# Performance work log

Measured on AMD Instinct MI355X. Metric: run time of the kernel, lower is better.

## Reference

```python
import jax, jax.numpy as jnp
import numpy as np

D_MODEL = 1024
N_HEADS = 16
HEAD_DIM = D_MODEL // N_HEADS


def setup_inputs() -> dict:
    key = jax.random.key(0)
    ks = jax.random.split(key, 5)
    q = jax.random.normal(ks[0], (2, 2048, D_MODEL), dtype=jnp.float32)
    Wq = jax.random.normal(ks[1], (D_MODEL, D_MODEL), dtype=jnp.float32) * (1.0 / np.sqrt(D_MODEL))
    bq = jax.random.normal(ks[2], (D_MODEL,), dtype=jnp.float32) * 0.01
    Wo = jax.random.normal(ks[3], (D_MODEL, D_MODEL), dtype=jnp.float32) * (1.0 / np.sqrt(D_MODEL))
    bo = jax.random.normal(ks[4], (D_MODEL,), dtype=jnp.float32) * 0.01
    return {"q": q, "Wq": Wq, "bq": bq, "Wo": Wo, "bo": bo}


def reference(q, Wq, bq, Wo, bo):
    bs, S, dim = q.shape
    # NOTE: original module (bug-faithfully) projects Q, K and V all with WQ.
    proj = q @ Wq.T + bq  # [B, S, D]
    h = proj.reshape(bs, S, N_HEADS, HEAD_DIM).transpose(0, 2, 1, 3)  # [B, H, S, Dh]
    qh, kh, vh = h, h, h
    scale = HEAD_DIM ** -0.5
    attn = jnp.einsum('bhqd,bhkd->bhqk', qh, kh) * scale  # [B, H, S, S]
    scores = jax.nn.softmax(attn, axis=-1)
    # dropout is identity in inference mode
    vals = jnp.einsum('bhqk,bhkd->bhqd', scores, vh)  # [B, H, S, Dh]
    vals = vals.transpose(0, 2, 1, 3).reshape(bs, S, dim)
    return vals @ Wo.T + bo
```

## Files before the change

### kernel.cpp

```cpp
#include <hip/hip_runtime.h>

#define D_MODEL 1024
#define N_HEADS 16
#define HEAD_DIM 64
#define SEQ 2048
#define BATCH 2
#define M_TOTAL (BATCH*SEQ)

typedef __bf16 bf16;
typedef __bf16 bf16x8 __attribute__((ext_vector_type(8)));
typedef __bf16 bf16x4 __attribute__((ext_vector_type(4)));
typedef float  floatx4 __attribute__((ext_vector_type(4)));

__device__ __forceinline__ void gl2lds16(const bf16* g, bf16* l) {
    __builtin_amdgcn_global_load_lds(
        (const __attribute__((address_space(1))) unsigned int*)g,
        (__attribute__((address_space(3))) unsigned int*)l, 16, 0, 0);
}

__global__ void cvt_all(const float* __restrict__ q, const float* __restrict__ Wq,
                        const float* __restrict__ Wo, bf16* __restrict__ qb,
                        bf16* __restrict__ wqb, bf16* __restrict__ wob) {
    int i = blockIdx.x * 256 + threadIdx.x;
    const float* src; bf16* dst; int off;
    if (i < 1048576)      { src = q;  dst = qb;  off = i; }
    else if (i < 1310720) { src = Wq; dst = wqb; off = i - 1048576; }
    else                  { src = Wo; dst = wob; off = i - 1310720; }
    float4 v = ((const float4*)src)[off];
    bf16x4 o;
    o[0] = (bf16)v.x; o[1] = (bf16)v.y; o[2] = (bf16)v.z; o[3] = (bf16)v.w;
    ((bf16x4*)dst)[off] = o;
}

template<int MODE>
__global__ __launch_bounds__(512)
void gemm_bt_bias_t(const bf16* __restrict__ A, const bf16* __restrict__ B,
                    const float* __restrict__ bias, void* __restrict__ Cout,
                    bf16* __restrict__ Cout2, int M, int N, int K)
{
    __shared__ __align__(16) bf16 As[2][128 * 32];
    __shared__ __align__(16) bf16 Bs[2][128 * 32];

    const int tid  = threadIdx.x;
    const int lane = tid & 63;
    const int wave = tid >> 6;
    const int quad = lane >> 4;
    const int l16  = lane & 15;
    const int m0   = blockIdx.y * 128;
    const int n0   = blockIdx.x * 128;
    const int wm   = (wave >> 2) * 64;
    const int wn   = (wave & 3) * 32;

    floatx4 acc[4][2];
#pragma unroll
    for (int i = 0; i < 4; i++)
#pragma unroll
        for (int j = 0; j < 2; j++) acc[i][j] = (floatx4){0.f, 0.f, 0.f, 0.f};

    const int srow = tid >> 2;
    const int sc   = (tid & 3) ^ ((srow >> 1) & 3);
    auto issue = [&](int buf, int k0) {
        gl2lds16(A + (size_t)(m0 + srow) * K + k0 + sc * 8, &As[buf][tid * 8]);
        gl2lds16(B + (size_t)(n0 + srow) * K + k0 + sc * 8, &Bs[buf][tid * 8]);
    };
    issue(0, 0);
    int buf = 0;
    for (int k0 = 0; k0 < K; k0 += 32, buf ^= 1) {
        __syncthreads();
        if (k0 + 32 < K) issue(buf ^ 1, k0 + 32);
        bf16x8 af[4], bfr[2];
#pragma unroll
        for (int i = 0; i < 4; i++) {
            int row = wm + i * 16 + l16;
            af[i] = *(const bf16x8*)&As[buf][row * 32 + ((quad ^ ((row >> 1) & 3)) * 8)];
        }
#pragma unroll
        for (int j = 0; j < 2; j++) {
            int row = wn + j * 16 + l16;
            bfr[j] = *(const bf16x8*)&Bs[buf][row * 32 + ((quad ^ ((row >> 1) & 3)) * 8)];
        }
#pragma unroll
        for (int i = 0; i < 4; i++)
#pragma unroll
            for (int j = 0; j < 2; j++)
                acc[i][j] = __builtin_amdgcn_mfma_f32_16x16x32_bf16(
                    af[i], bfr[j], acc[i][j], 0, 0, 0);
    }

    if constexpr (MODE == 0) {
        float* C = (float*)Cout;
#pragma unroll
        for (int j = 0; j < 2; j++) {
            int col  = n0 + wn + j * 16 + l16;
            float bv = bias[col];
#pragma unroll
            for (int i = 0; i < 4; i++) {
                int rbase = m0 + wm + i * 16 + quad * 4;
#pragma unroll
                for (int r = 0; r < 4; r++)
                    C[(size_t)(rbase + r) * N + col] = acc[i][j][r] + bv;
            }
        }
    } else {
        bf16* Cb = (bf16*)Cout;
#pragma unroll
        for (int j = 0; j < 2; j++) {
            int col = n0 + wn + j * 16 + l16;
            int h   = col >> 6, d = col & 63;
            float bv = bias[col];
#pragma unroll
            for (int i = 0; i < 4; i++) {
                int rbase = m0 + wm + i * 16 + quad * 4;
                int b  = rbase >> 11;
                int s0 = rbase & 2047;
                bf16x4 o4;
#pragma unroll
                for (int r = 0; r < 4; r++) {
                    float v = acc[i][j][r] + bv;
                    o4[r] = (bf16)v;
                    Cb[(((size_t)(b * N_HEADS + h) * SEQ + (s0 + r)) << 6) + d] = (bf16)v;
                }
                *(bf16x4*)&Cout2[((size_t)(b * N_HEADS + h) * 64 + d) * SEQ + s0] = o4;
            }
        }
    }
}

__global__ __launch_bounds__(256)
void flash_attn(const bf16* __restrict__ projbf, const bf16* __restrict__ projT,
                bf16* __restrict__ vals)
{
    __shared__ __align__(16) bf16 Ks[2][128 * 64];
    __shared__ __align__(16) bf16 Vt[2][64 * 128];
    __shared__ __align__(16) bf16 Pt[128 * 40];

    const int tid  = threadIdx.x;
    const int lane = tid & 63;
    const int wave = tid >> 6;
    const int quad = lane >> 4;
    const int l16  = lane & 15;
    const int q0   = blockIdx.x * 128;
    const int bh   = blockIdx.y;
    const bf16* hK  = projbf + (size_t)bh * SEQ * 64;
    const bf16* hVt = projT  + (size_t)bh * 64 * SEQ;
    const int wq0  = wave * 32;

    bf16x8 qf[2][2];
#pragma unroll
    for (int nb = 0; nb < 2; nb++)
#pragma unroll
        for (int ks = 0; ks < 2; ks++)
            qf[nb][ks] = *(const bf16x8*)(hK + (size_t)(q0 + wq0 + nb * 16 + l16) * 64
                                          + ks * 32 + quad * 8);

    floatx4 oacc[4][2];
#pragma unroll
    for (int mb = 0; mb < 4; mb++)
#pragma unroll
        for (int nb = 0; nb < 2; nb++) oacc[mb][nb] = (floatx4){0.f, 0.f, 0.f, 0.f};
    float lsum[2] = {0.f, 0.f};

    auto issue = [&](int buf, int k0) {
#pragma unroll
        for (int it = 0; it < 4; it++) {
            int row = it * 32 + (tid >> 3);
            int c   = (tid & 7) ^ (row & 7);
            gl2lds16(hK + (size_t)(k0 + row) * 64 + c * 8,
                     &Ks[buf][it * 2048 + tid * 8]);
        }
#pragma unroll
        for (int it = 0; it < 4; it++) {
            int row = it * 16 + (tid >> 4);
            int c   = (tid & 15) ^ (row & 15);
            gl2lds16(hVt + (size_t)row * SEQ + k0 + c * 8,
                     &Vt[buf][it * 2048 + tid * 8]);
        }
    };
    issue(0, 0);
    int buf = 0;
    for (int k0 = 0; k0 < SEQ; k0 += 128, buf ^= 1) {
        __syncthreads();
        if (k0 + 128 < SEQ) issue(buf ^ 1, k0 + 128);

#pragma unroll
        for (int ck = 0; ck < 4; ck++) {
#pragma unroll
            for (int kb = 0; kb < 2; kb++) {
                int krow = ck * 32 + kb * 16 + l16;
                bf16x8 kf0 = *(const bf16x8*)&Ks[buf][krow * 64 + ((quad ^ (krow & 7)) * 8)];
                bf16x8 kf1 = *(const bf16x8*)&Ks[buf][krow * 64 + (((4 + quad) ^ (krow & 7)) * 8)];
                floatx4 sacc[2];
#pragma unroll
                for (int nb = 0; nb < 2; nb++) {
                    sacc[nb] = __builtin_amdgcn_mfma_f32_16x16x32_bf16(
                        kf0, qf[nb][0], (floatx4){0.f, 0.f, 0.f, 0.f}, 0, 0, 0);
                    sacc[nb] = __builtin_amdgcn_mfma_f32_16x16x32_bf16(
                        kf1, qf[nb][1], sacc[nb], 0, 0, 0);
                }
#pragma unroll
                for (int nb = 0; nb < 2; nb++) {
                    bf16x4 p4; float ps = 0.f;
#pragma unroll
                    for (int r = 0; r < 4; r++) {
                        float p = __expf(sacc[nb][r] * 0.125f - 16.0f);
                        p4[r] = (bf16)p; ps += p;
                    }
                    lsum[nb] += ps;
                    *(bf16x4*)&Pt[(wq0 + nb * 16 + l16) * 40 + kb * 16 + quad * 4] = p4;
                }
            }
            bf16x8 pf[2];
#pragma unroll
            for (int nb = 0; nb < 2; nb++)
                pf[nb] = *(const bf16x8*)&Pt[(wq0 + nb * 16 + l16) * 40 + quad * 8];
#pragma unroll
            for (int mb = 0; mb < 4; mb++) {
                int vrow = mb * 16 + l16;
                bf16x8 vf = *(const bf16x8*)&Vt[buf][vrow * 128
                                                + (((ck * 4 + quad) ^ (vrow & 15)) * 8)];
#pragma unroll
                for (int nb = 0; nb < 2; nb++)
                    oacc[mb][nb] = __builtin_amdgcn_mfma_f32_16x16x32_bf16(
                        vf, pf[nb], oacc[mb][nb], 0, 0, 0);
            }
        }
    }

#pragma unroll
    for (int nb = 0; nb < 2; nb++) {
        lsum[nb] += __shfl_xor(lsum[nb], 16);
        lsum[nb] += __shfl_xor(lsum[nb], 32);
    }
    const int b = bh >> 4, h = bh & 15;
#pragma unroll
    for (int nb = 0; nb < 2; nb++) {
        float rinv = 1.0f / lsum[nb];
        int q = q0 + wq0 + nb * 16 + l16;
#pragma unroll
        for (int mb = 0; mb < 4; mb++) {
            bf16x4 o4;
#pragma unroll
            for (int r = 0; r < 4; r++) o4[r] = (bf16)(oacc[mb][nb][r] * rinv);
            *(bf16x4*)&vals[((size_t)b * SEQ + q) * D_MODEL + h * 64 + mb * 16 + quad * 4] = o4;
        }
    }
}

extern "C" void kernel_launch(void* const* d_in, const int* in_sizes, int n_in,
                              void* d_out, int out_size, void* d_ws, size_t ws_size,
                              hipStream_t stream)
{
    const float* q  = (const float*)d_in[0];
    const float* Wq = (const float*)d_in[1];
    const float* bq = (const float*)d_in[2];
    const float* Wo = (const float*)d_in[3];
    const float* bo = (const float*)d_in[4];
    float* out = (float*)d_out;

    char* ws = (char*)d_ws;
    bf16* qbf    = (bf16*)(ws);
    bf16* Wqbf   = (bf16*)(ws + (size_t)( 8 << 20));
    bf16* Wobf   = (bf16*)(ws + (size_t)(10 << 20));
    bf16* projbf = (bf16*)(ws + (size_t)(12 << 20));
    bf16* projT  = (bf16*)(ws + (size_t)(20 << 20));
    bf16* valsb  = (bf16*)(ws + (size_t)(28 << 20));

    cvt_all<<<6144, 256, 0, stream>>>(q, Wq, Wo, qbf, Wqbf, Wobf);

    gemm_bt_bias_t<1><<<dim3(8, 32), 512, 0, stream>>>(qbf, Wqbf, bq, (void*)projbf,
                                                       projT, M_TOTAL, D_MODEL, D_MODEL);

    flash_attn<<<dim3(SEQ / 128, BATCH * N_HEADS), 256, 0, stream>>>(projbf, projT, valsb);

    gemm_bt_bias_t<0><<<dim3(8, 32), 512, 0, stream>>>(valsb, Wobf, bo, (void*)out,
                                                       nullptr, M_TOTAL, D_MODEL, D_MODEL);
}
```

Before: 179.9 us.

## Stage transposed projection store through LDS and remap attention grid for L2 locality

The projection GEMM epilogue now writes the transposed V copy by first placing the tile in the shared memory buffer with an XOR swizzle, then emitting coalesced 16-byte row stores instead of strided 8-byte stores. The flash attention launch becomes a 1D grid whose block index is remapped so that blocks of the same head land on the same XCD under round-robin dispatch, improving L2 reuse of K/V. The epilogue adds two barriers and reuses the GEMM LDS buffers.

After: 170.6 us. 1.05x faster.

```diff
diff --git a/kernel.cpp b/kernel.cpp
--- a/kernel.cpp
+++ b/kernel.cpp
@@ -38,8 +38,9 @@
                     const float* __restrict__ bias, void* __restrict__ Cout,
                     bf16* __restrict__ Cout2, int M, int N, int K)
 {
-    __shared__ __align__(16) bf16 As[2][128 * 32];
-    __shared__ __align__(16) bf16 Bs[2][128 * 32];
+    __shared__ __align__(16) bf16 smem[16384];
+    bf16* As = smem;
+    bf16* Bs = smem + 8192;
 
     const int tid  = threadIdx.x;
     const int lane = tid & 63;
@@ -60,8 +61,8 @@
     const int srow = tid >> 2;
     const int sc   = (tid & 3) ^ ((srow >> 1) & 3);
     auto issue = [&](int buf, int k0) {
-        gl2lds16(A + (size_t)(m0 + srow) * K + k0 + sc * 8, &As[buf][tid * 8]);
-        gl2lds16(B + (size_t)(n0 + srow) * K + k0 + sc * 8, &Bs[buf][tid * 8]);
+        gl2lds16(A + (size_t)(m0 + srow) * K + k0 + sc * 8, &As[buf * 4096 + tid * 8]);
+        gl2lds16(B + (size_t)(n0 + srow) * K + k0 + sc * 8, &Bs[buf * 4096 + tid * 8]);
     };
     issue(0, 0);
     int buf = 0;
@@ -72,12 +73,12 @@
 #pragma unroll
         for (int i = 0; i < 4; i++) {
             int row = wm + i * 16 + l16;
-            af[i] = *(const bf16x8*)&As[buf][row * 32 + ((quad ^ ((row >> 1) & 3)) * 8)];
+            af[i] = *(const bf16x8*)&As[buf * 4096 + row * 32 + ((quad ^ ((row >> 1) & 3)) * 8)];
         }
 #pragma unroll
         for (int j = 0; j < 2; j++) {
             int row = wn + j * 16 + l16;
-            bfr[j] = *(const bf16x8*)&Bs[buf][row * 32 + ((quad ^ ((row >> 1) & 3)) * 8)];
+            bfr[j] = *(const bf16x8*)&Bs[buf * 4096 + row * 32 + ((quad ^ ((row >> 1) & 3)) * 8)];
         }
 #pragma unroll
         for (int i = 0; i < 4; i++)
@@ -103,6 +104,7 @@
         }
     } else {
         bf16* Cb = (bf16*)Cout;
+        bf16x4 tile[4][2];
 #pragma unroll
         for (int j = 0; j < 2; j++) {
             int col = n0 + wn + j * 16 + l16;
@@ -113,14 +115,36 @@
                 int rbase = m0 + wm + i * 16 + quad * 4;
                 int b  = rbase >> 11;
                 int s0 = rbase & 2047;
-                bf16x4 o4;
 #pragma unroll
                 for (int r = 0; r < 4; r++) {
                     float v = acc[i][j][r] + bv;
-                    o4[r] = (bf16)v;
+                    tile[i][j][r] = (bf16)v;
                     Cb[(((size_t)(b * N_HEADS + h) * SEQ + (s0 + r)) << 6) + d] = (bf16)v;
                 }
-                *(bf16x4*)&Cout2[((size_t)(b * N_HEADS + h) * 64 + d) * SEQ + s0] = o4;
+            }
+        }
+        __syncthreads();
+#pragma unroll
+        for (int j = 0; j < 2; j++) {
+            int dL = wn + j * 16 + l16;
+#pragma unroll
+            for (int i = 0; i < 4; i++) {
+                int s0 = wm + i * 16 + quad * 4;
+                *(bf16x4*)&smem[dL * 128 + (((s0 >> 3) ^ (dL & 15)) * 8) + (s0 & 7)] =
+                    tile[i][j];
+            }
+        }
+        __syncthreads();
+        {
+            int dL   = tid >> 2;
+            int hg   = (n0 + dL) >> 6, d = (n0 + dL) & 63;
+            int b    = m0 >> 11, sbase = m0 & 2047;
+            bf16* dstrow = Cout2 + ((size_t)(b * N_HEADS + hg) * 64 + d) * SEQ + sbase;
+#pragma unroll
+            for (int cc = 0; cc < 4; cc++) {
+                int c    = (tid & 3) * 4 + cc;
+                int phys = c ^ (dL & 15);
+                *(bf16x8*)(dstrow + c * 8) = *(const bf16x8*)&smem[dL * 128 + phys * 8];
             }
         }
     }
@@ -139,8 +163,9 @@
     const int wave = tid >> 6;
     const int quad = lane >> 4;
     const int l16  = lane & 15;
-    const int q0   = blockIdx.x * 128;
-    const int bh   = blockIdx.y;
+    const int lin  = blockIdx.x;
+    const int bh   = (lin & 7) * 4 + (lin >> 7);
+    const int q0   = ((lin >> 3) & 15) * 128;
     const bf16* hK  = projbf + (size_t)bh * SEQ * 64;
     const bf16* hVt = projT  + (size_t)bh * 64 * SEQ;
     const int wq0  = wave * 32;
@@ -270,7 +295,7 @@
     gemm_bt_bias_t<1><<<dim3(8, 32), 512, 0, stream>>>(qbf, Wqbf, bq, (void*)projbf,
                                                        projT, M_TOTAL, D_MODEL, D_MODEL);
 
-    flash_attn<<<dim3(SEQ / 128, BATCH * N_HEADS), 256, 0, stream>>>(projbf, projT, valsb);
+    flash_attn<<<512, 256, 0, stream>>>(projbf, projT, valsb);
 
     gemm_bt_bias_t<0><<<dim3(8, 32), 512, 0, stream>>>(valsb, Wobf, bo, (void*)out,
                                                        nullptr, M_TOTAL, D_MODEL, D_MODEL);
```
